# Kernel tuning notes

Hardware: AMD Instinct MI355X
Metric: run time of the kernel (lower is better)

Reference implementation:

```python
import jax, jax.numpy as jnp
import numpy as np

ROPE_BASE = 10000.0

def _rope(x):
    # x: (B, T, H, hd); rotate-half RoPE
    B, T, H, hd = x.shape
    half = hd // 2
    inv_freq = 1.0 / (ROPE_BASE ** (jnp.arange(half, dtype=jnp.float32) / half))
    ang = jnp.arange(T, dtype=jnp.float32)[:, None] * inv_freq[None, :]  # (T, half)
    cos = jnp.cos(ang)[None, :, None, :]
    sin = jnp.sin(ang)[None, :, None, :]
    x1, x2 = x[..., :half], x[..., half:]
    return jnp.concatenate([x1 * cos - x2 * sin, x1 * sin + x2 * cos], axis=-1)

def setup_inputs() -> dict:
    key = jax.random.key(0)
    k1, k2, k3 = jax.random.split(key, 3)
    B, T, D = 4, 2048, 2048
    x = jax.random.normal(k1, (B, T, D), dtype=jnp.float32)
    attn_mask = jnp.ones((B, T), dtype=bool)
    w_qkv = jax.random.normal(k2, (3 * D, D), dtype=jnp.float32) * (D ** -0.5)
    w_out = jax.random.normal(k3, (D, D), dtype=jnp.float32) * (D ** -0.5)
    return {"x": x, "attn_mask": attn_mask, "is_causal": 1, "w_qkv": w_qkv, "w_out": w_out}

def reference(x, attn_mask, is_causal, w_qkv, w_out):
    B, T, D = x.shape
    H = 16
    hd = D // H
    qkv = jnp.einsum('btd,ed->bte', x, w_qkv)  # (B, T, 3D)
    q, k, v = jnp.split(qkv, 3, axis=2)
    q = _rope(q.reshape(B, T, H, hd))
    k = _rope(k.reshape(B, T, H, hd))
    v = v.reshape(B, T, H, hd)
    scale = 1.0 / jnp.sqrt(jnp.float32(hd))
    scores = jnp.einsum('bqhd,bkhd->bhqk', q, k) * scale  # (B, H, T, T)
    if is_causal:
        mask = jnp.tril(jnp.ones((T, T), dtype=bool))[None, None]
    else:
        mask = attn_mask[:, None, None, :]  # (B,1,1,T)
    scores = jnp.where(mask, scores, jnp.finfo(scores.dtype).min)
    attn = jax.nn.softmax(scores, axis=-1)
    y = jnp.einsum('bhqk,bkhd->bqhd', attn, v).reshape(B, T, D)
    return jnp.einsum('btd,ed->bte', y, w_out)
```

## Files before the change

### kernel.cpp

```cpp
#include <hip/hip_runtime.h>
#include <stdint.h>
#include <stddef.h>

typedef float f32x4 __attribute__((ext_vector_type(4)));
typedef __bf16 bf16x8 __attribute__((ext_vector_type(8)));
typedef short s16x4 __attribute__((ext_vector_type(4)));

#define DEVI static __device__ __forceinline__

DEVI float bf2f(unsigned short u) {
  unsigned int x = ((unsigned int)u) << 16;
  float f;
  __builtin_memcpy(&f, &x, 4);
  return f;
}
DEVI unsigned short f2bf(float f) {
  unsigned int x;
  __builtin_memcpy(&x, &f, 4);
  unsigned int r = (x + 0x7fffu + ((x >> 16) & 1u)) >> 16;
  return (unsigned short)r;
}

DEVI void async16(const void* g, void* l) {
  __builtin_amdgcn_global_load_lds((__attribute__((address_space(1))) void*)g,
                                   (__attribute__((address_space(3))) void*)l,
                                   16, 0, 0);
}

#define BAR_VM(N)                                               \
  do {                                                          \
    asm volatile("s_waitcnt vmcnt(" #N ")" ::: "memory");       \
    __builtin_amdgcn_s_barrier();                               \
    __builtin_amdgcn_sched_barrier(0);                          \
  } while (0)

#define BAR_LGKM()                                          \
  do {                                                      \
    asm volatile("s_waitcnt lgkmcnt(0)" ::: "memory");      \
    __builtin_amdgcn_s_barrier();                           \
    __builtin_amdgcn_sched_barrier(0);                      \
  } while (0)

__global__ __launch_bounds__(256) void cvt3(const float* __restrict__ x,
                                            const float* __restrict__ wq,
                                            const float* __restrict__ wo,
                                            unsigned short* __restrict__ xb,
                                            unsigned short* __restrict__ wqb,
                                            unsigned short* __restrict__ wob) {
  const int n1 = 16777216, n2 = 12582912;
  int i = (blockIdx.x * 256 + threadIdx.x) * 4;
  const float* src;
  unsigned short* dst;
  int off;
  if (i < n1) {
    src = x; dst = xb; off = i;
  } else if (i < n1 + n2) {
    src = wq; dst = wqb; off = i - n1;
  } else {
    src = wo; dst = wob; off = i - n1 - n2;
  }
  float4 v = *(const float4*)(src + off);
  s16x4 o;
  o[0] = (short)f2bf(v.x);
  o[1] = (short)f2bf(v.y);
  o[2] = (short)f2bf(v.z);
  o[3] = (short)f2bf(v.w);
  *(s16x4*)(dst + off) = o;
}

__global__ __launch_bounds__(256) void rope_table(float* __restrict__ tab) {
  int idx = blockIdx.x * 256 + threadIdx.x;
  if (idx >= 2048 * 64) return;
  int tt = idx >> 6, j = idx & 63;
  float inv = powf(10000.0f, -(float)j * (1.0f / 64.0f));
  float ang = (float)tt * inv;
  tab[tt * 128 + j] = cosf(ang);
  tab[tt * 128 + 64 + j] = sinf(ang);
}

__global__ __launch_bounds__(256) void rope_apply(unsigned short* __restrict__ Qg,
                                                  unsigned short* __restrict__ Kg,
                                                  const float* __restrict__ tab) {
  const float S2 = 0.0883883476483184f * 1.44269504088896341f;
  int idx = blockIdx.x * 256 + threadIdx.x;
  int j4 = idx & 15;
  int tt = (idx >> 4) & 2047;
  int bh = idx >> 15;
  size_t base = ((size_t)bh * 2048 + tt) * 128;
  f32x4 c4 = *(const f32x4*)(tab + tt * 128 + j4 * 4);
  f32x4 s4 = *(const f32x4*)(tab + tt * 128 + 64 + j4 * 4);
  s16x4 q1 = *(const s16x4*)(Qg + base + j4 * 4);
  s16x4 q2 = *(const s16x4*)(Qg + base + 64 + j4 * 4);
  s16x4 k1 = *(const s16x4*)(Kg + base + j4 * 4);
  s16x4 k2 = *(const s16x4*)(Kg + base + 64 + j4 * 4);
  s16x4 o1, o2, p1, p2;
#pragma unroll
  for (int r = 0; r < 4; ++r) {
    float c = c4[r], s = s4[r];
    float a = bf2f((unsigned short)q1[r]), b2 = bf2f((unsigned short)q2[r]);
    o1[r] = (short)f2bf((a * c - b2 * s) * S2);
    o2[r] = (short)f2bf((a * s + b2 * c) * S2);
    float ka = bf2f((unsigned short)k1[r]), kb = bf2f((unsigned short)k2[r]);
    p1[r] = (short)f2bf(ka * c - kb * s);
    p2[r] = (short)f2bf(ka * s + kb * c);
  }
  *(s16x4*)(Qg + base + j4 * 4) = o1;
  *(s16x4*)(Qg + base + 64 + j4 * 4) = o2;
  *(s16x4*)(Kg + base + j4 * 4) = p1;
  *(s16x4*)(Kg + base + 64 + j4 * 4) = p2;
}

template <int EPI>
__global__ __launch_bounds__(512) void gemm256(const unsigned short* __restrict__ A,
                                               const unsigned short* __restrict__ B,
                                               float* __restrict__ C, int M, int N, int K,
                                               unsigned short* __restrict__ Q,
                                               unsigned short* __restrict__ Kk,
                                               unsigned short* __restrict__ VT) {
  __shared__ __attribute__((aligned(128))) unsigned short Al[2][2][8192];
  __shared__ __attribute__((aligned(128))) unsigned short Bl[2][2][8192];
  const int t = threadIdx.x;
  const int lane = t & 63;
  const int w = t >> 6, wr = w >> 2, wc = w & 3;
  const int g = lane >> 4, lr = lane & 15;

  const int id = blockIdx.y * gridDim.x + blockIdx.x;
  const int mt = M >> 8, nt = N >> 8;
  const int xcd = id & 7;
  const int local = id >> 3;
  const int rm = mt >> 2, rn = nt >> 1;
  const int bm = ((xcd & 3) * rm + (local % rm)) * 256;
  const int bn = ((xcd >> 2) * rn + (local / rm)) * 256;

  const unsigned short* aptr = A + (size_t)bm * K;
  const unsigned short* bptr = B + (size_t)bn * K;

  const int srow = t >> 3;
  const int sslot = (t & 7) ^ (srow & 7);

#define STG(arr, mat, p, h, kt)                                                   \
  do {                                                                            \
    const unsigned short* _s =                                                    \
        (mat) + (size_t)((h) * 128 + srow) * K + (size_t)(kt) * 64 + sslot * 8;   \
    async16(_s, &arr[p][h][t * 8]);                                               \
    async16(_s + (size_t)64 * K, &arr[p][h][t * 8 + 4096]);                       \
  } while (0)

  const int u0 = ((g ^ (lr & 7)) * 8) + lr * 64;
  const int u1 = (((4 + g) ^ (lr & 7)) * 8) + lr * 64;

#define LDA_(p, mh)                                                               \
  _Pragma("unroll") for (int mf = 0; mf < 4; ++mf) {                              \
    af[mf][0] = *(const bf16x8*)&Al[p][wr][(mh) * 4096 + mf * 1024 + u0];         \
    af[mf][1] = *(const bf16x8*)&Al[p][wr][(mh) * 4096 + mf * 1024 + u1];         \
  }
#define LDB_(dst, p, nh)                                                          \
  _Pragma("unroll") for (int nf = 0; nf < 2; ++nf) {                              \
    dst[nf][0] = *(const bf16x8*)&Bl[p][wc >> 1][(wc & 1) * 4096 + (nh) * 2048 +  \
                                                 nf * 1024 + u0];                 \
    dst[nf][1] = *(const bf16x8*)&Bl[p][wc >> 1][(wc & 1) * 4096 + (nh) * 2048 +  \
                                                 nf * 1024 + u1];                 \
  }
#define MMA_(bsrc, mh, nh)                                                        \
  __builtin_amdgcn_s_setprio(1);                                                  \
  _Pragma("unroll") for (int mf = 0; mf < 4; ++mf)                                \
      _Pragma("unroll") for (int nf = 0; nf < 2; ++nf) {                          \
    acc[(mh) * 4 + mf][(nh) * 2 + nf] = __builtin_amdgcn_mfma_f32_16x16x32_bf16(  \
        af[mf][0], bsrc[nf][0], acc[(mh) * 4 + mf][(nh) * 2 + nf], 0, 0, 0);      \
    acc[(mh) * 4 + mf][(nh) * 2 + nf] = __builtin_amdgcn_mfma_f32_16x16x32_bf16(  \
        af[mf][1], bsrc[nf][1], acc[(mh) * 4 + mf][(nh) * 2 + nf], 0, 0, 0);      \
  }                                                                               \
  __builtin_amdgcn_s_setprio(0);
#define BARR() __builtin_amdgcn_s_barrier();

  f32x4 acc[8][4] = {};
  bf16x8 af[4][2], bfrA[2][2], bfrB[2][2];

  STG(Al, aptr, 0, 0, 0);
  STG(Al, aptr, 0, 1, 0);
  STG(Bl, bptr, 0, 0, 0);
  STG(Bl, bptr, 0, 1, 0);
  STG(Bl, bptr, 1, 0, 1);
  STG(Bl, bptr, 1, 1, 1);
  asm volatile("s_waitcnt vmcnt(4)" ::: "memory");
  __builtin_amdgcn_s_barrier();

  const int NITER = K >> 7;
  for (int i = 0; i < NITER; ++i) {
    const bool G = (i + 1 < NITER);
    const int t1 = 2 * i + 1, t2 = 2 * i + 2, t3 = 2 * i + 3;

    LDA_(0, 0);
    LDB_(bfrA, 0, 0);
    STG(Al, aptr, 1, 0, t1);
    STG(Al, aptr, 1, 1, t1);
    BARR();
    MMA_(bfrA, 0, 0);
    BARR();
    LDB_(bfrB, 0, 1);
    BARR();
    MMA_(bfrB, 0, 1);
    BARR();
    LDA_(0, 1);
    BARR();
    MMA_(bfrB, 1, 1);
    BARR();
    if (G) {
      STG(Bl, bptr, 0, 0, t2);
      asm volatile("s_waitcnt vmcnt(2)" ::: "memory");
    } else {
      asm volatile("s_waitcnt vmcnt(0)" ::: "memory");
    }
    BARR();
    MMA_(bfrA, 1, 0);
    BARR();
    LDA_(1, 0);
    LDB_(bfrA, 1, 0);
    if (G) STG(Bl, bptr, 0, 1, t2);
    BARR();
    MMA_(bfrA, 0, 0);
    BARR();
    LDB_(bfrB, 1, 1);
    if (G) STG(Al, aptr, 0, 0, t2);
    BARR();
    MMA_(bfrB, 0, 1);
    BARR();
    LDA_(1, 1);
    if (G) STG(Al, aptr, 0, 1, t2);
    BARR();
    MMA_(bfrB, 1, 1);
    BARR();
    if (G) {
      STG(Bl, bptr, 1, 0, t3);
      STG(Bl, bptr, 1, 1, t3);
      asm volatile("s_waitcnt vmcnt(4)" ::: "memory");
    }
    BARR();
    MMA_(bfrA, 1, 0);
    BARR();
  }
#undef STG
#undef LDA_
#undef LDB_
#undef MMA_
#undef BARR

  if (EPI == 0) {
#pragma unroll
    for (int mp = 0; mp < 8; ++mp) {
      int m0 = bm + wr * 128 + (mp >> 2) * 64 + (mp & 3) * 16 + g * 4;
#pragma unroll
      for (int nfi = 0; nfi < 4; ++nfi) {
        int n = bn + wc * 64 + (nfi >> 1) * 32 + (nfi & 1) * 16 + lr;
#pragma unroll
        for (int r = 0; r < 4; ++r) C[(size_t)(m0 + r) * N + n] = acc[mp][nfi][r];
      }
    }
  } else {
    const int bi = bm >> 11;
    const int tbase = bm & 2047;
#pragma unroll
    for (int nfi = 0; nfi < 4; ++nfi) {
      int e = bn + wc * 64 + (nfi >> 1) * 32 + (nfi & 1) * 16 + lr;
      int region = e >> 11;
      int e2 = e & 2047;
      int h = e2 >> 7, d = e2 & 127;
      int bh = bi * 16 + h;
#pragma unroll
      for (int mp = 0; mp < 8; ++mp) {
        int trow = tbase + wr * 128 + (mp >> 2) * 64 + (mp & 3) * 16 + g * 4;
        if (region == 2) {
          s16x4 pk;
#pragma unroll
          for (int r = 0; r < 4; ++r) pk[r] = (short)f2bf(acc[mp][nfi][r]);
          *(s16x4*)(VT + ((size_t)bh * 128 + d) * 2048 + trow) = pk;
        } else {
          unsigned short* dst = (region == 0) ? Q : Kk;
#pragma unroll
          for (int r = 0; r < 4; ++r)
            dst[((size_t)bh * 2048 + trow + r) * 128 + d] = f2bf(acc[mp][nfi][r]);
        }
      }
    }
  }
}

__global__ __launch_bounds__(1024) void flash_attn(const unsigned short* __restrict__ Qg,
                                                   const unsigned short* __restrict__ Kg,
                                                   const unsigned short* __restrict__ VTg,
                                                   unsigned short* __restrict__ Yg,
                                                   const int* __restrict__ iscausal,
                                                   const unsigned char* __restrict__ amask) {
  __shared__ __attribute__((aligned(128))) unsigned short Ks[2][64 * 128];
  __shared__ __attribute__((aligned(128))) unsigned short Vs[2][128 * 64];
  __shared__ __attribute__((aligned(128))) unsigned short Ps[16][16 * 72];

  const int t = threadIdx.x, lane = t & 63, w = t >> 6;
  const int g = lane >> 4, lr = lane & 15;
  const int id = blockIdx.x;
  const int xcd = id & 7, j5 = id >> 3;
  const int rr = j5 >> 3;
  const int qbi = (rr & 1) ? (rr >> 1) : (7 - (rr >> 1));
  const int bh = xcd * 8 + (j5 & 7);
  const int b = bh >> 4;
  const int qb = qbi * 256;
  const int causal = iscausal[0] != 0;
  const int nt = causal ? (4 * qbi + 4) : 32;

  const unsigned short* qrow = Qg + ((size_t)bh * 2048 + qb + w * 16 + lr) * 128;
  bf16x8 qf[4];
#pragma unroll
  for (int ds = 0; ds < 4; ++ds) qf[ds] = *(const bf16x8*)(qrow + ds * 32 + g * 8);

  const unsigned short* Kbase = Kg + (size_t)bh * 2048 * 128;
  const unsigned short* Vbase = VTg + (size_t)bh * 128 * 2048;

  const int rK = t >> 4, sK = (t & 15) ^ (rK & 15);
  const int rV = t >> 3, sV = (t & 7) ^ (rV & 7);

#define STAGE(KT, P)                                                              \
  do {                                                                            \
    const int _kv = (KT) * 64;                                                    \
    async16(Kbase + (size_t)(_kv + rK) * 128 + sK * 8, &Ks[P][t * 8]);            \
    async16(Vbase + (size_t)rV * 2048 + _kv + sV * 8, &Vs[P][t * 8]);             \
  } while (0)

  unsigned int oi[4] = {0x3F803F80u, 0x3F803F80u, 0x3F803F80u, 0x3F803F80u};
  bf16x8 ones;
  __builtin_memcpy(&ones, oi, 16);

  f32x4 acc[8] = {};
  f32x4 accl = {0.f, 0.f, 0.f, 0.f};
  float mrow[4] = {-1e30f, -1e30f, -1e30f, -1e30f};

  STAGE(0, 0);

  for (int kt = 0; kt < nt; ++kt) {
    const int p = kt & 1;
    const int kv0 = kt * 64;
    if (kt + 1 < nt) {
      STAGE(kt + 1, p ^ 1);
      BAR_VM(2);
    } else {
      BAR_VM(0);
    }

    const int qw = qb + w * 16;
    const bool active = !causal || (kv0 <= qw + 15);
    if (active) {
      f32x4 s[4] = {};
      __builtin_amdgcn_s_setprio(1);
#pragma unroll
      for (int cf = 0; cf < 4; ++cf)
#pragma unroll
        for (int ds = 0; ds < 4; ++ds) {
          bf16x8 kf = *(const bf16x8*)(&Ks[p][(cf * 16 + lr) * 128 + (((ds * 4 + g) ^ lr) * 8)]);
          s[cf] = __builtin_amdgcn_mfma_f32_16x16x32_bf16(qf[ds], kf, s[cf], 0, 0, 0);
        }
      __builtin_amdgcn_s_setprio(0);

      const int q0 = qw + g * 4;
      if (causal) {
        if (kv0 + 63 > qw) {
#pragma unroll
          for (int cf = 0; cf < 4; ++cf) {
            int kvg = kv0 + cf * 16 + lr;
#pragma unroll
            for (int r = 0; r < 4; ++r)
              if (kvg > q0 + r) s[cf][r] = -1e30f;
          }
        }
      } else {
#pragma unroll
        for (int cf = 0; cf < 4; ++cf) {
          int kvg = kv0 + cf * 16 + lr;
          if (!amask[(size_t)b * 2048 + kvg]) {
#pragma unroll
            for (int r = 0; r < 4; ++r) s[cf][r] = -1e30f;
          }
        }
      }

      f32x4 lm;
#pragma unroll
      for (int r = 0; r < 4; ++r)
        lm[r] = fmaxf(fmaxf(s[0][r], s[1][r]), fmaxf(s[2][r], s[3][r]));
      bool ok = true;
#pragma unroll
      for (int r = 0; r < 4; ++r) ok = ok && (lm[r] <= mrow[r] + 8.0f);
      if (!__all(ok)) {
        f32x4 mx = lm;
#pragma unroll
        for (int off = 8; off >= 1; off >>= 1)
#pragma unroll
          for (int r = 0; r < 4; ++r) mx[r] = fmaxf(mx[r], __shfl_xor(mx[r], off));
#pragma unroll
        for (int r = 0; r < 4; ++r) {
          float mn = fmaxf(mrow[r], mx[r]);
          float corr = exp2f(mrow[r] - mn);
          mrow[r] = mn;
          accl[r] *= corr;
#pragma unroll
          for (int jf = 0; jf < 8; ++jf) acc[jf][r] *= corr;
        }
      }

#pragma unroll
      for (int cf = 0; cf < 4; ++cf)
#pragma unroll
        for (int r = 0; r < 4; ++r) s[cf][r] = exp2f(s[cf][r] - mrow[r]);

      unsigned short* Pw = &Ps[w][0];
#pragma unroll
      for (int cf = 0; cf < 4; ++cf)
#pragma unroll
        for (int r = 0; r < 4; ++r) Pw[(g * 4 + r) * 72 + cf * 16 + lr] = f2bf(s[cf][r]);
      asm volatile("s_waitcnt lgkmcnt(0)" ::: "memory");
      __builtin_amdgcn_sched_barrier(0);

      bf16x8 pa0 = *(const bf16x8*)(Pw + lr * 72 + g * 8);
      bf16x8 pa1 = *(const bf16x8*)(Pw + lr * 72 + 32 + g * 8);

      accl = __builtin_amdgcn_mfma_f32_16x16x32_bf16(pa0, ones, accl, 0, 0, 0);
      accl = __builtin_amdgcn_mfma_f32_16x16x32_bf16(pa1, ones, accl, 0, 0, 0);

      __builtin_amdgcn_s_setprio(1);
#pragma unroll
      for (int jf = 0; jf < 8; ++jf) {
        bf16x8 v0 = *(const bf16x8*)(&Vs[p][(jf * 16 + lr) * 64 + ((g ^ (lr & 7)) * 8)]);
        bf16x8 v1 = *(const bf16x8*)(&Vs[p][(jf * 16 + lr) * 64 + (((4 + g) ^ (lr & 7)) * 8)]);
        acc[jf] = __builtin_amdgcn_mfma_f32_16x16x32_bf16(pa0, v0, acc[jf], 0, 0, 0);
        acc[jf] = __builtin_amdgcn_mfma_f32_16x16x32_bf16(pa1, v1, acc[jf], 0, 0, 0);
      }
      __builtin_amdgcn_s_setprio(0);
    }

    BAR_LGKM();
  }
#undef STAGE

  const int h = bh & 15;
  float rl[4];
#pragma unroll
  for (int r = 0; r < 4; ++r) rl[r] = __builtin_amdgcn_rcpf(accl[r]);
#pragma unroll
  for (int jf = 0; jf < 8; ++jf)
#pragma unroll
    for (int r = 0; r < 4; ++r) {
      int tt = qb + w * 16 + g * 4 + r;
      Yg[((size_t)b * 2048 + tt) * 2048 + h * 128 + jf * 16 + lr] = f2bf(acc[jf][r] * rl[r]);
    }
}

extern "C" void kernel_launch(void* const* d_in, const int* in_sizes, int n_in, void* d_out,
                              int out_size, void* d_ws, size_t ws_size, hipStream_t stream) {
  const float* x = (const float*)d_in[0];
  const unsigned char* amask = (const unsigned char*)d_in[1];
  const int* iscausal = (const int*)d_in[2];
  const float* wqkv = (const float*)d_in[3];
  const float* wout = (const float*)d_in[4];
  float* out = (float*)d_out;

  const size_t MT = 8192, D = 2048, ND = 6144;
  unsigned short* xb = (unsigned short*)d_ws;
  unsigned short* wqkvb = xb + MT * D;
  unsigned short* woutb = wqkvb + ND * D;
  unsigned short* q = woutb + D * D;
  unsigned short* k = q + MT * D;
  unsigned short* vt = k + MT * D;
  unsigned short* y = vt + MT * D;
  float* tab = (float*)(y + MT * D);
  if (ws_size < (size_t)(100663296) * 2 + 2048 * 128 * 4) return;

  cvt3<<<dim3(32768), dim3(256), 0, stream>>>(x, wqkv, wout, xb, wqkvb, woutb);
  rope_table<<<dim3(512), dim3(256), 0, stream>>>(tab);
  gemm256<1><<<dim3(24, 32), dim3(512), 0, stream>>>(xb, wqkvb, nullptr, 8192, 6144, 2048, q, k, vt);
  rope_apply<<<dim3(8192), dim3(256), 0, stream>>>(q, k, tab);
  flash_attn<<<dim3(512), dim3(1024), 0, stream>>>(q, k, vt, y, iscausal, amask);
  gemm256<0><<<dim3(8, 32), dim3(512), 0, stream>>>(y, woutb, out, 8192, 2048, 2048, nullptr,
                                                    nullptr, nullptr);
}
```

Measured before the change: 442.0 us.

## Fuse Q RoPE into attention prologue and merge rope table into convert kernel

```diff
diff --git a/kernel.cpp b/kernel.cpp
--- a/kernel.cpp
+++ b/kernel.cpp
@@ -46,9 +46,20 @@
                                             const float* __restrict__ wo,
                                             unsigned short* __restrict__ xb,
                                             unsigned short* __restrict__ wqb,
-                                            unsigned short* __restrict__ wob) {
-  const int n1 = 16777216, n2 = 12582912;
+                                            unsigned short* __restrict__ wob,
+                                            float* __restrict__ tab) {
+  const int n1 = 16777216, n2 = 12582912, n3 = 4194304;
   int i = (blockIdx.x * 256 + threadIdx.x) * 4;
+  if (i >= n1 + n2 + n3) {
+    int idx = i / 4 - (n1 + n2 + n3) / 4;
+    if (idx >= 2048 * 64) return;
+    int tt = idx >> 6, j = idx & 63;
+    float inv = powf(10000.0f, -(float)j * (1.0f / 64.0f));
+    float ang = (float)tt * inv;
+    tab[tt * 128 + j] = cosf(ang);
+    tab[tt * 128 + 64 + j] = sinf(ang);
+    return;
+  }
   const float* src;
   unsigned short* dst;
   int off;
@@ -68,20 +79,8 @@
   *(s16x4*)(dst + off) = o;
 }
 
-__global__ __launch_bounds__(256) void rope_table(float* __restrict__ tab) {
-  int idx = blockIdx.x * 256 + threadIdx.x;
-  if (idx >= 2048 * 64) return;
-  int tt = idx >> 6, j = idx & 63;
-  float inv = powf(10000.0f, -(float)j * (1.0f / 64.0f));
-  float ang = (float)tt * inv;
-  tab[tt * 128 + j] = cosf(ang);
-  tab[tt * 128 + 64 + j] = sinf(ang);
-}
-
-__global__ __launch_bounds__(256) void rope_apply(unsigned short* __restrict__ Qg,
-                                                  unsigned short* __restrict__ Kg,
-                                                  const float* __restrict__ tab) {
-  const float S2 = 0.0883883476483184f * 1.44269504088896341f;
+__global__ __launch_bounds__(256) void rope_apply_k(unsigned short* __restrict__ Kg,
+                                                    const float* __restrict__ tab) {
   int idx = blockIdx.x * 256 + threadIdx.x;
   int j4 = idx & 15;
   int tt = (idx >> 4) & 2047;
@@ -89,23 +88,16 @@
   size_t base = ((size_t)bh * 2048 + tt) * 128;
   f32x4 c4 = *(const f32x4*)(tab + tt * 128 + j4 * 4);
   f32x4 s4 = *(const f32x4*)(tab + tt * 128 + 64 + j4 * 4);
-  s16x4 q1 = *(const s16x4*)(Qg + base + j4 * 4);
-  s16x4 q2 = *(const s16x4*)(Qg + base + 64 + j4 * 4);
   s16x4 k1 = *(const s16x4*)(Kg + base + j4 * 4);
   s16x4 k2 = *(const s16x4*)(Kg + base + 64 + j4 * 4);
-  s16x4 o1, o2, p1, p2;
+  s16x4 p1, p2;
 #pragma unroll
   for (int r = 0; r < 4; ++r) {
     float c = c4[r], s = s4[r];
-    float a = bf2f((unsigned short)q1[r]), b2 = bf2f((unsigned short)q2[r]);
-    o1[r] = (short)f2bf((a * c - b2 * s) * S2);
-    o2[r] = (short)f2bf((a * s + b2 * c) * S2);
     float ka = bf2f((unsigned short)k1[r]), kb = bf2f((unsigned short)k2[r]);
     p1[r] = (short)f2bf(ka * c - kb * s);
     p2[r] = (short)f2bf(ka * s + kb * c);
   }
-  *(s16x4*)(Qg + base + j4 * 4) = o1;
-  *(s16x4*)(Qg + base + 64 + j4 * 4) = o2;
   *(s16x4*)(Kg + base + j4 * 4) = p1;
   *(s16x4*)(Kg + base + 64 + j4 * 4) = p2;
 }
@@ -290,7 +282,8 @@
                                                    const unsigned short* __restrict__ VTg,
                                                    unsigned short* __restrict__ Yg,
                                                    const int* __restrict__ iscausal,
-                                                   const unsigned char* __restrict__ amask) {
+                                                   const unsigned char* __restrict__ amask,
+                                                   const float* __restrict__ tab) {
   __shared__ __attribute__((aligned(128))) unsigned short Ks[2][64 * 128];
   __shared__ __attribute__((aligned(128))) unsigned short Vs[2][128 * 64];
   __shared__ __attribute__((aligned(128))) unsigned short Ps[16][16 * 72];
@@ -307,10 +300,29 @@
   const int causal = iscausal[0] != 0;
   const int nt = causal ? (4 * qbi + 4) : 32;
 
-  const unsigned short* qrow = Qg + ((size_t)bh * 2048 + qb + w * 16 + lr) * 128;
+  const float S2 = 0.0883883476483184f * 1.44269504088896341f;
+  const int qpos = qb + w * 16 + lr;
+  const unsigned short* qrow = Qg + ((size_t)bh * 2048 + qpos) * 128;
+  const float* trow = tab + (size_t)qpos * 128;
+  bf16x8 qraw[4];
+#pragma unroll
+  for (int ds = 0; ds < 4; ++ds) qraw[ds] = *(const bf16x8*)(qrow + ds * 32 + g * 8);
   bf16x8 qf[4];
-#pragma unroll
-  for (int ds = 0; ds < 4; ++ds) qf[ds] = *(const bf16x8*)(qrow + ds * 32 + g * 8);
+  {
+    unsigned short* tq = (unsigned short*)qraw;
+    unsigned short* oq = (unsigned short*)qf;
+#pragma unroll
+    for (int half = 0; half < 2; ++half)
+#pragma unroll
+      for (int e = 0; e < 8; ++e) {
+        int j = half * 32 + g * 8 + e;
+        float c = trow[j], s = trow[64 + j];
+        float a = bf2f(tq[half * 8 + e]);
+        float b2 = bf2f(tq[(half + 2) * 8 + e]);
+        oq[half * 8 + e] = f2bf((a * c - b2 * s) * S2);
+        oq[(half + 2) * 8 + e] = f2bf((a * s + b2 * c) * S2);
+      }
+  }
 
   const unsigned short* Kbase = Kg + (size_t)bh * 2048 * 128;
   const unsigned short* Vbase = VTg + (size_t)bh * 128 * 2048;
@@ -472,11 +484,10 @@
   float* tab = (float*)(y + MT * D);
   if (ws_size < (size_t)(100663296) * 2 + 2048 * 128 * 4) return;
 
-  cvt3<<<dim3(32768), dim3(256), 0, stream>>>(x, wqkv, wout, xb, wqkvb, woutb);
-  rope_table<<<dim3(512), dim3(256), 0, stream>>>(tab);
+  cvt3<<<dim3(33280), dim3(256), 0, stream>>>(x, wqkv, wout, xb, wqkvb, woutb, tab);
   gemm256<1><<<dim3(24, 32), dim3(512), 0, stream>>>(xb, wqkvb, nullptr, 8192, 6144, 2048, q, k, vt);
-  rope_apply<<<dim3(8192), dim3(256), 0, stream>>>(q, k, tab);
-  flash_attn<<<dim3(512), dim3(1024), 0, stream>>>(q, k, vt, y, iscausal, amask);
+  rope_apply_k<<<dim3(8192), dim3(256), 0, stream>>>(k, tab);
+  flash_attn<<<dim3(512), dim3(1024), 0, stream>>>(q, k, vt, y, iscausal, amask, tab);
   gemm256<0><<<dim3(8, 32), dim3(512), 0, stream>>>(y, woutb, out, 8192, 2048, 2048, nullptr,
                                                     nullptr, nullptr);
 }
```

Result: no change. 440.4 us, median of 2 (-0.4%).
